# Kernel tuning notes

Hardware: AMD Instinct MI355X
Metric: run time of the kernel (lower is better)

## Reference

```python
import jax, jax.numpy as jnp
import numpy as np

B, N, DIN, DOUT = 4, 4096, 512, 128
NEG_INF = -1.0e9  # matches torch's -1000000000.0 fill


def setup_inputs() -> dict:
    key = jax.random.key(0)
    k1, k2, k3, k4 = jax.random.split(key, 4)
    x = jax.random.normal(k1, (B, N, DIN), dtype=jnp.float32)
    adj = (jax.random.uniform(k2, (N, N)) < 0.004).astype(jnp.float32)
    # xavier_uniform with gain=sqrt(2) for weights
    lim_w = float(np.sqrt(2.0) * np.sqrt(6.0 / (DIN + DOUT)))
    weights = jax.random.uniform(k3, (DIN, DOUT), jnp.float32, -lim_w, lim_w)
    # xavier_uniform (gain=1) for a: shape [2*DOUT, 1]
    lim_a = float(np.sqrt(6.0 / (2 * DOUT + 1)))
    a = jax.random.uniform(k4, (2 * DOUT, 1), jnp.float32, -lim_a, lim_a)
    return {"x": x, "adj": adj, "weights": weights, "a": a}


def reference(x, adj, weights, a):
    d = weights.shape[1]
    a_src = a[:d]   # [D, 1]
    a_dst = a[d:]   # [D, 1]

    def per_graph(xs):  # xs: [N, DIN]
        wh = xs @ weights                      # [N, D]
        e = wh @ a_src + (wh @ a_dst).T        # [N,1] + [1,N] -> [N,N]
        e = jnp.where(e > 0, e, 0.01 * e)      # LeakyReLU(0.01)
        att = jax.nn.softmax(jnp.where(adj > 0, e, NEG_INF), axis=1)
        out = att @ wh                          # [N, D]
        return adj @ out                        # sparse-adj mm (dense here)

    return jax.nn.relu(jax.vmap(per_graph)(x))  # act = ReLU
```

## Files before the change

### kernel.cpp

```cpp
#include <hip/hip_runtime.h>
#include <cstdint>
#include <cstddef>

#define BATCH 4
#define NNODE 4096
#define DIN   512
#define DOUT  128
#define CAP   64

typedef __attribute__((ext_vector_type(8))) short bf16x8;
typedef __attribute__((ext_vector_type(4))) float f32x4;
typedef __attribute__((ext_vector_type(4))) unsigned short us4;

static __device__ __forceinline__ unsigned short f2bf_rne(float f) {
    union { float f; uint32_t u; } v; v.f = f;
    uint32_t u = v.u;
    uint32_t r = u + 0x7FFFu + ((u >> 16) & 1u);
    return (unsigned short)(r >> 16);
}
static __device__ __forceinline__ float bf2f(unsigned short h) {
    union { float f; uint32_t u; } v; v.u = ((uint32_t)h) << 16;
    return v.f;
}

__global__ __launch_bounds__(256) void k_pre(const float* __restrict__ adj,
                                             const float* __restrict__ W,
                                             int* __restrict__ nbr_cnt,
                                             int* __restrict__ nbr_idx,
                                             unsigned short* __restrict__ Wt) {
    int t = threadIdx.x;
    if (blockIdx.x < NNODE) {
        __shared__ int scnt;
        int row = blockIdx.x;
        if (t == 0) scnt = 0;
        __syncthreads();
        const float4* p = (const float4*)(adj + (size_t)row * NNODE) + t * 4;
        unsigned mask = 0;
#pragma unroll
        for (int q = 0; q < 4; ++q) {
            float4 v = p[q];
            mask |= (v.x > 0.f ? 1u : 0u) << (q*4+0);
            mask |= (v.y > 0.f ? 1u : 0u) << (q*4+1);
            mask |= (v.z > 0.f ? 1u : 0u) << (q*4+2);
            mask |= (v.w > 0.f ? 1u : 0u) << (q*4+3);
        }
        int cnt = __popc(mask);
        int base = cnt ? atomicAdd(&scnt, cnt) : 0;
        int cbase = t * 16;
        while (mask) {
            int b = __ffs(mask) - 1;
            mask &= mask - 1;
            if (base < CAP) nbr_idx[row * CAP + base] = cbase + b;
            ++base;
        }
        __syncthreads();
        if (t == 0) nbr_cnt[row] = scnt > CAP ? CAP : scnt;
    } else {
        int wb = blockIdx.x - NNODE;
        int i0 = wb * 1024;
#pragma unroll
        for (int r = 0; r < 4; ++r) {
            int i = i0 + r * 256 + t;
            int n = i >> 9;
            int k = i & (DIN - 1);
            Wt[i] = f2bf_rne(W[(size_t)k * DOUT + n]);
        }
    }
}

__global__ __launch_bounds__(256) void k_wh(const float* __restrict__ x,
                                            const unsigned short* __restrict__ Wt,
                                            const float* __restrict__ a,
                                            unsigned short* __restrict__ wh,
                                            float* __restrict__ sv,
                                            float* __restrict__ dvv,
                                            float* __restrict__ colpart) {
    __shared__ float lacc[3][8][64][4];
    int t = threadIdx.x;
    int w = t >> 6;
    int l = t & 63;
    int rowbase = blockIdx.x * 16;
    int row = rowbase + (l & 15);
    int kq = w * 128 + ((l >> 4) << 3);
    f32x4 acc[8] = {};
    const float* xrow = x + (size_t)row * DIN + kq;
    const unsigned short* wb = Wt + kq;
#pragma unroll
    for (int ks = 0; ks < 4; ++ks) {
        float4 a0 = *(const float4*)(xrow + ks * 32);
        float4 a1 = *(const float4*)(xrow + ks * 32 + 4);
        float af[8] = {a0.x,a0.y,a0.z,a0.w,a1.x,a1.y,a1.z,a1.w};
        bf16x8 ah, al;
#pragma unroll
        for (int i = 0; i < 8; ++i) {
            unsigned short hh = f2bf_rne(af[i]);
            ah[i] = (short)hh;
            al[i] = (short)f2bf_rne(af[i] - bf2f(hh));
        }
#pragma unroll
        for (int ni = 0; ni < 8; ++ni) {
            bf16x8 b = *(const bf16x8*)(wb + (size_t)(ni*16 + (l & 15)) * DIN + ks * 32);
            acc[ni] = __builtin_amdgcn_mfma_f32_16x16x32_bf16(ah, b, acc[ni], 0, 0, 0);
            acc[ni] = __builtin_amdgcn_mfma_f32_16x16x32_bf16(al, b, acc[ni], 0, 0, 0);
        }
    }
    if (w > 0) {
#pragma unroll
        for (int ni = 0; ni < 8; ++ni)
            *(f32x4*)&lacc[w-1][ni][l][0] = acc[ni];
    }
    __syncthreads();
    if (w == 0) {
#pragma unroll
        for (int ni = 0; ni < 8; ++ni) {
            acc[ni] += *(const f32x4*)&lacc[0][ni][l][0];
            acc[ni] += *(const f32x4*)&lacc[1][ni][l][0];
            acc[ni] += *(const f32x4*)&lacc[2][ni][l][0];
        }
        float sp[4] = {0,0,0,0}, dp[4] = {0,0,0,0};
#pragma unroll
        for (int ni = 0; ni < 8; ++ni) {
            int col = ni*16 + (l & 15);
            float as = a[col], ad = a[DOUT + col];
#pragma unroll
            for (int r = 0; r < 4; ++r) {
                sp[r] += acc[ni][r] * as;
                dp[r] += acc[ni][r] * ad;
            }
        }
#pragma unroll
        for (int off = 1; off <= 8; off <<= 1) {
#pragma unroll
            for (int r = 0; r < 4; ++r) {
                sp[r] += __shfl_xor(sp[r], off, 64);
                dp[r] += __shfl_xor(dp[r], off, 64);
            }
        }
        int row4 = rowbase + ((l >> 4) << 2);
        if ((l & 15) == 0) {
#pragma unroll
            for (int r = 0; r < 4; ++r) {
                sv[row4 + r] = sp[r];
                dvv[row4 + r] = dp[r];
            }
        }
#pragma unroll
        for (int ni = 0; ni < 8; ++ni) {
            int col = ni*16 + (l & 15);
            float rs = acc[ni][0] + acc[ni][1] + acc[ni][2] + acc[ni][3];
            rs += __shfl_xor(rs, 16, 64);
            rs += __shfl_xor(rs, 32, 64);
            if (l < 16) colpart[(size_t)blockIdx.x * DOUT + ni*16 + l] = rs;
#pragma unroll
            for (int r = 0; r < 4; ++r)
                wh[(size_t)(row4 + r) * DOUT + col] = f2bf_rne(acc[ni][r]);
        }
    }
}

__global__ __launch_bounds__(256) void k_att(const unsigned short* __restrict__ wh,
                                             const float* __restrict__ s,
                                             const float* __restrict__ dv,
                                             const int* __restrict__ nbr_cnt,
                                             const int* __restrict__ nbr_idx,
                                             const float* __restrict__ colpart,
                                             unsigned short* __restrict__ out) {
    int bswz = (int)(((blockIdx.x & 7) << 9) | (blockIdx.x >> 3));
    int gid = bswz * 4 + (threadIdx.x >> 6);
    int l = threadIdx.x & 63;
    int b = gid >> 12;
    int i = gid & (NNODE - 1);
    int bb = b << 12;
    int c = nbr_cnt[i];
    int j = (l < c) ? nbr_idx[i * CAP + l] : 0;
    float p = 0.f;
    if (l < c) {
        float ev = s[gid] + dv[bb + j];
        ev = ev > 0.f ? ev : 0.01f * ev;
        p = __expf(ev);
    }
    float den = p;
#pragma unroll
    for (int off = 32; off >= 1; off >>= 1) den += __shfl_xor(den, off, 64);
    int half = l >> 5;
    int lc = l & 31;
    float4 acc = {0.f, 0.f, 0.f, 0.f};
    if (c > 0) {
        for (int jj = 0; jj < c; jj += 8) {
            int s0 = jj + half,     s1 = jj + 2 + half;
            int s2 = jj + 4 + half, s3 = jj + 6 + half;
            int jv0 = __shfl(j, s0, 64); float pv0 = __shfl(p, s0, 64);
            int jv1 = __shfl(j, s1, 64); float pv1 = __shfl(p, s1, 64);
            int jv2 = __shfl(j, s2, 64); float pv2 = __shfl(p, s2, 64);
            int jv3 = __shfl(j, s3, 64); float pv3 = __shfl(p, s3, 64);
            us4 v0 = *((const us4*)(wh + (size_t)(bb + jv0) * DOUT) + lc);
            us4 v1 = *((const us4*)(wh + (size_t)(bb + jv1) * DOUT) + lc);
            us4 v2 = *((const us4*)(wh + (size_t)(bb + jv2) * DOUT) + lc);
            us4 v3 = *((const us4*)(wh + (size_t)(bb + jv3) * DOUT) + lc);
            acc.x += pv0*bf2f(v0[0]) + pv1*bf2f(v1[0]) + pv2*bf2f(v2[0]) + pv3*bf2f(v3[0]);
            acc.y += pv0*bf2f(v0[1]) + pv1*bf2f(v1[1]) + pv2*bf2f(v2[1]) + pv3*bf2f(v3[1]);
            acc.z += pv0*bf2f(v0[2]) + pv1*bf2f(v1[2]) + pv2*bf2f(v2[2]) + pv3*bf2f(v3[2]);
            acc.w += pv0*bf2f(v0[3]) + pv1*bf2f(v1[3]) + pv2*bf2f(v2[3]) + pv3*bf2f(v3[3]);
        }
        acc.x += __shfl_xor(acc.x, 32, 64);
        acc.y += __shfl_xor(acc.y, 32, 64);
        acc.z += __shfl_xor(acc.z, 32, 64);
        acc.w += __shfl_xor(acc.w, 32, 64);
        float inv = 1.f / den;
        acc.x *= inv; acc.y *= inv; acc.z *= inv; acc.w *= inv;
    } else {
        const float inv_n = 1.f / (float)NNODE;
        for (int gg = 0; gg < 256; ++gg) {
            const float* cp = colpart + (size_t)((b << 8) + gg) * DOUT + lc*4;
            acc.x += cp[0]; acc.y += cp[1]; acc.z += cp[2]; acc.w += cp[3];
        }
        acc.x *= inv_n; acc.y *= inv_n; acc.z *= inv_n; acc.w *= inv_n;
    }
    if (half == 0) {
        us4 o;
        o[0] = f2bf_rne(acc.x); o[1] = f2bf_rne(acc.y);
        o[2] = f2bf_rne(acc.z); o[3] = f2bf_rne(acc.w);
        *((us4*)(out + (size_t)gid * DOUT) + lc) = o;
    }
}

__global__ __launch_bounds__(256) void k_agg(const unsigned short* __restrict__ out,
                                             const int* __restrict__ nbr_cnt,
                                             const int* __restrict__ nbr_idx,
                                             float* __restrict__ y) {
    int bswz = (int)(((blockIdx.x & 7) << 9) | (blockIdx.x >> 3));
    int gid = bswz * 4 + (threadIdx.x >> 6);
    int l = threadIdx.x & 63;
    int b = gid >> 12;
    int i = gid & (NNODE - 1);
    int bb = b << 12;
    int c = nbr_cnt[i];
    int j = (l < c) ? nbr_idx[i * CAP + l] : 0;
    float wt = (l < c) ? 1.f : 0.f;
    int half = l >> 5;
    int lc = l & 31;
    float4 acc = {0.f, 0.f, 0.f, 0.f};
    for (int jj = 0; jj < c; jj += 8) {
        int s0 = jj + half,     s1 = jj + 2 + half;
        int s2 = jj + 4 + half, s3 = jj + 6 + half;
        int jv0 = __shfl(j, s0, 64); float pv0 = __shfl(wt, s0, 64);
        int jv1 = __shfl(j, s1, 64); float pv1 = __shfl(wt, s1, 64);
        int jv2 = __shfl(j, s2, 64); float pv2 = __shfl(wt, s2, 64);
        int jv3 = __shfl(j, s3, 64); float pv3 = __shfl(wt, s3, 64);
        us4 v0 = *((const us4*)(out + (size_t)(bb + jv0) * DOUT) + lc);
        us4 v1 = *((const us4*)(out + (size_t)(bb + jv1) * DOUT) + lc);
        us4 v2 = *((const us4*)(out + (size_t)(bb + jv2) * DOUT) + lc);
        us4 v3 = *((const us4*)(out + (size_t)(bb + jv3) * DOUT) + lc);
        acc.x += pv0*bf2f(v0[0]) + pv1*bf2f(v1[0]) + pv2*bf2f(v2[0]) + pv3*bf2f(v3[0]);
        acc.y += pv0*bf2f(v0[1]) + pv1*bf2f(v1[1]) + pv2*bf2f(v2[1]) + pv3*bf2f(v3[1]);
        acc.z += pv0*bf2f(v0[2]) + pv1*bf2f(v1[2]) + pv2*bf2f(v2[2]) + pv3*bf2f(v3[2]);
        acc.w += pv0*bf2f(v0[3]) + pv1*bf2f(v1[3]) + pv2*bf2f(v2[3]) + pv3*bf2f(v3[3]);
    }
    acc.x += __shfl_xor(acc.x, 32, 64);
    acc.y += __shfl_xor(acc.y, 32, 64);
    acc.z += __shfl_xor(acc.z, 32, 64);
    acc.w += __shfl_xor(acc.w, 32, 64);
    acc.x = fmaxf(acc.x, 0.f); acc.y = fmaxf(acc.y, 0.f);
    acc.z = fmaxf(acc.z, 0.f); acc.w = fmaxf(acc.w, 0.f);
    if (half == 0)
        *((float4*)(y + (size_t)gid * DOUT) + lc) = acc;
}

extern "C" void kernel_launch(void* const* d_in, const int* in_sizes, int n_in,
                              void* d_out, int out_size, void* d_ws, size_t ws_size,
                              hipStream_t stream) {
    const float* x   = (const float*)d_in[0];
    const float* adj = (const float*)d_in[1];
    const float* W   = (const float*)d_in[2];
    const float* a   = (const float*)d_in[3];
    float* y = (float*)d_out;

    char* ws = (char*)d_ws;
    size_t o = 0;
    int*            nbr_cnt = (int*)(ws + o);            o += (size_t)NNODE * 4;
    int*            nbr_idx = (int*)(ws + o);            o += (size_t)NNODE * CAP * 4;
    unsigned short* Wt      = (unsigned short*)(ws + o); o += (size_t)DOUT * DIN * 2;
    unsigned short* wh      = (unsigned short*)(ws + o); o += (size_t)BATCH * NNODE * DOUT * 2;
    float*          sv      = (float*)(ws + o);          o += (size_t)BATCH * NNODE * 4;
    float*          dvv     = (float*)(ws + o);          o += (size_t)BATCH * NNODE * 4;
    float*          colpart = (float*)(ws + o);          o += (size_t)1024 * DOUT * 4;
    unsigned short* outbuf  = (unsigned short*)(ws + o); o += (size_t)BATCH * NNODE * DOUT * 2;

    k_pre<<<NNODE + 64, 256, 0, stream>>>(adj, W, nbr_cnt, nbr_idx, Wt);
    k_wh <<<1024, 256, 0, stream>>>(x, Wt, a, wh, sv, dvv, colpart);
    k_att<<<(BATCH*NNODE)/4, 256, 0, stream>>>(wh, sv, dvv, nbr_cnt, nbr_idx, colpart, outbuf);
    k_agg<<<(BATCH*NNODE)/4, 256, 0, stream>>>(outbuf, nbr_cnt, nbr_idx, y);
}
```

Before: 162.6 us.

## Fuse adjacency scan with Wh GEMM in one interleaved kernel

Splits the weight transpose into its own small kernel and merges the adjacency neighbor-list build with the x@W GEMM into one launch. Every fifth block does a GEMM tile and the other four scan one adjacency row, so bandwidth-bound and MFMA work run at the same time. The GEMM epilogue now spreads the wh/colpart writes across all four waves. The neighbor compaction replaces the shared atomic with a deterministic prefix scan, which costs many extra barriers per row block.

```diff
diff --git a/kernel.cpp b/kernel.cpp
--- a/kernel.cpp
+++ b/kernel.cpp
@@ -8,6 +8,8 @@
 #define DOUT  128
 #define CAP   64
 
+#define WH_BLOCKS 1024
+
 typedef __attribute__((ext_vector_type(8))) short bf16x8;
 typedef __attribute__((ext_vector_type(4))) float f32x4;
 typedef __attribute__((ext_vector_type(4))) unsigned short us4;
@@ -23,17 +25,118 @@
     return v.f;
 }
 
-__global__ __launch_bounds__(256) void k_pre(const float* __restrict__ adj,
-                                             const float* __restrict__ W,
-                                             int* __restrict__ nbr_cnt,
-                                             int* __restrict__ nbr_idx,
-                                             unsigned short* __restrict__ Wt) {
+__global__ __launch_bounds__(256) void k_wt(const float* __restrict__ W,
+                                            unsigned short* __restrict__ Wt) {
     int t = threadIdx.x;
-    if (blockIdx.x < NNODE) {
-        __shared__ int scnt;
-        int row = blockIdx.x;
-        if (t == 0) scnt = 0;
+    int i0 = blockIdx.x * 1024;
+#pragma unroll
+    for (int r = 0; r < 4; ++r) {
+        int i = i0 + r * 256 + t;
+        int n = i >> 9;
+        int k = i & (DIN - 1);
+        Wt[i] = f2bf_rne(W[(size_t)k * DOUT + n]);
+    }
+}
+
+__global__ __launch_bounds__(256) void k_main(const float* __restrict__ x,
+                                              const float* __restrict__ adj,
+                                              const unsigned short* __restrict__ Wt,
+                                              const float* __restrict__ a,
+                                              unsigned short* __restrict__ wh,
+                                              float* __restrict__ sv,
+                                              float* __restrict__ dvv,
+                                              float* __restrict__ colpart,
+                                              int* __restrict__ nbr_cnt,
+                                              int* __restrict__ nbr_idx) {
+    __shared__ float lacc[4][8][64][4];
+    __shared__ int pref[256];
+    int t = threadIdx.x;
+    int w = t >> 6;
+    int l = t & 63;
+    int bid = blockIdx.x;
+
+    if (bid % 5 == 0) {
+        int rowbase = (bid / 5) * 16;
+        int row = rowbase + (l & 15);
+        int kq = w * 128 + ((l >> 4) << 3);
+        f32x4 acc[8] = {};
+        const float* xrow = x + (size_t)row * DIN + kq;
+        const unsigned short* wb = Wt + kq;
+#pragma unroll
+        for (int ks = 0; ks < 4; ++ks) {
+            float4 a0 = *(const float4*)(xrow + ks * 32);
+            float4 a1 = *(const float4*)(xrow + ks * 32 + 4);
+            float af[8] = {a0.x,a0.y,a0.z,a0.w,a1.x,a1.y,a1.z,a1.w};
+            bf16x8 ah, al;
+#pragma unroll
+            for (int i = 0; i < 8; ++i) {
+                unsigned short hh = f2bf_rne(af[i]);
+                ah[i] = (short)hh;
+                al[i] = (short)f2bf_rne(af[i] - bf2f(hh));
+            }
+#pragma unroll
+            for (int ni = 0; ni < 8; ++ni) {
+                bf16x8 b = *(const bf16x8*)(wb + (size_t)(ni*16 + (l & 15)) * DIN + ks * 32);
+                acc[ni] = __builtin_amdgcn_mfma_f32_16x16x32_bf16(ah, b, acc[ni], 0, 0, 0);
+                acc[ni] = __builtin_amdgcn_mfma_f32_16x16x32_bf16(al, b, acc[ni], 0, 0, 0);
+            }
+        }
+#pragma unroll
+        for (int ni = 0; ni < 8; ++ni)
+            *(f32x4*)&lacc[w][ni][l][0] = acc[ni];
         __syncthreads();
+
+        int row4 = rowbase + ((l >> 4) << 2);
+#pragma unroll
+        for (int q = 0; q < 2; ++q) {
+            int ni = w * 2 + q;
+            f32x4 sum = *(const f32x4*)&lacc[0][ni][l][0];
+            sum += *(const f32x4*)&lacc[1][ni][l][0];
+            sum += *(const f32x4*)&lacc[2][ni][l][0];
+            sum += *(const f32x4*)&lacc[3][ni][l][0];
+            int col = ni*16 + (l & 15);
+#pragma unroll
+            for (int r = 0; r < 4; ++r)
+                wh[(size_t)(row4 + r) * DOUT + col] = f2bf_rne(sum[r]);
+            float rs = sum[0] + sum[1] + sum[2] + sum[3];
+            rs += __shfl_xor(rs, 16, 64);
+            rs += __shfl_xor(rs, 32, 64);
+            if (l < 16) colpart[(size_t)(bid / 5) * DOUT + ni*16 + l] = rs;
+        }
+        if (w == 0) {
+            float sp[4] = {0,0,0,0}, dp[4] = {0,0,0,0};
+#pragma unroll
+            for (int ni = 0; ni < 8; ++ni) {
+                f32x4 sum = *(const f32x4*)&lacc[0][ni][l][0];
+                sum += *(const f32x4*)&lacc[1][ni][l][0];
+                sum += *(const f32x4*)&lacc[2][ni][l][0];
+                sum += *(const f32x4*)&lacc[3][ni][l][0];
+                int col = ni*16 + (l & 15);
+                float as = a[col], ad = a[DOUT + col];
+#pragma unroll
+                for (int r = 0; r < 4; ++r) {
+                    sp[r] += sum[r] * as;
+                    dp[r] += sum[r] * ad;
+                }
+            }
+#pragma unroll
+            for (int off = 1; off <= 8; off <<= 1) {
+#pragma unroll
+                for (int r = 0; r < 4; ++r) {
+                    sp[r] += __shfl_xor(sp[r], off, 64);
+                    dp[r] += __shfl_xor(dp[r], off, 64);
+                }
+            }
+            if ((l & 15) == 0) {
+#pragma unroll
+                for (int r = 0; r < 4; ++r) {
+                    sv[row4 + r] = sp[r];
+                    dvv[row4 + r] = dp[r];
+                }
+            }
+        }
+    } else {
+        int row = bid - bid / 5 - 1;
         const float4* p = (const float4*)(adj + (size_t)row * NNODE) + t * 4;
         unsigned mask = 0;
 #pragma unroll
@@ -45,7 +148,17 @@
             mask |= (v.w > 0.f ? 1u : 0u) << (q*4+3);
         }
         int cnt = __popc(mask);
-        int base = cnt ? atomicAdd(&scnt, cnt) : 0;
+        pref[t] = cnt;
+        __syncthreads();
+        for (int off = 1; off < 256; off <<= 1) {
+            int v = pref[t];
+            int add = (t >= off) ? pref[t - off] : 0;
+            __syncthreads();
+            pref[t] = v + add;
+            __syncthreads();
+        }
+        int total = pref[255];
+        int base = pref[t] - cnt;
         int cbase = t * 16;
         while (mask) {
             int b = __ffs(mask) - 1;
@@ -53,108 +166,7 @@
             if (base < CAP) nbr_idx[row * CAP + base] = cbase + b;
             ++base;
         }
-        __syncthreads();
-        if (t == 0) nbr_cnt[row] = scnt > CAP ? CAP : scnt;
-    } else {
-        int wb = blockIdx.x - NNODE;
-        int i0 = wb * 1024;
-#pragma unroll
-        for (int r = 0; r < 4; ++r) {
-            int i = i0 + r * 256 + t;
-            int n = i >> 9;
-            int k = i & (DIN - 1);
-            Wt[i] = f2bf_rne(W[(size_t)k * DOUT + n]);
-        }
-    }
-}
-
-__global__ __launch_bounds__(256) void k_wh(const float* __restrict__ x,
-                                            const unsigned short* __restrict__ Wt,
-                                            const float* __restrict__ a,
-                                            unsigned short* __restrict__ wh,
-                                            float* __restrict__ sv,
-                                            float* __restrict__ dvv,
-                                            float* __restrict__ colpart) {
-    __shared__ float lacc[3][8][64][4];
-    int t = threadIdx.x;
-    int w = t >> 6;
-    int l = t & 63;
-    int rowbase = blockIdx.x * 16;
-    int row = rowbase + (l & 15);
-    int kq = w * 128 + ((l >> 4) << 3);
-    f32x4 acc[8] = {};
-    const float* xrow = x + (size_t)row * DIN + kq;
-    const unsigned short* wb = Wt + kq;
-#pragma unroll
-    for (int ks = 0; ks < 4; ++ks) {
-        float4 a0 = *(const float4*)(xrow + ks * 32);
-        float4 a1 = *(const float4*)(xrow + ks * 32 + 4);
-        float af[8] = {a0.x,a0.y,a0.z,a0.w,a1.x,a1.y,a1.z,a1.w};
-        bf16x8 ah, al;
-#pragma unroll
-        for (int i = 0; i < 8; ++i) {
-            unsigned short hh = f2bf_rne(af[i]);
-            ah[i] = (short)hh;
-            al[i] = (short)f2bf_rne(af[i] - bf2f(hh));
-        }
-#pragma unroll
-        for (int ni = 0; ni < 8; ++ni) {
-            bf16x8 b = *(const bf16x8*)(wb + (size_t)(ni*16 + (l & 15)) * DIN + ks * 32);
-            acc[ni] = __builtin_amdgcn_mfma_f32_16x16x32_bf16(ah, b, acc[ni], 0, 0, 0);
-            acc[ni] = __builtin_amdgcn_mfma_f32_16x16x32_bf16(al, b, acc[ni], 0, 0, 0);
-        }
-    }
-    if (w > 0) {
-#pragma unroll
-        for (int ni = 0; ni < 8; ++ni)
-            *(f32x4*)&lacc[w-1][ni][l][0] = acc[ni];
-    }
-    __syncthreads();
-    if (w == 0) {
-#pragma unroll
-        for (int ni = 0; ni < 8; ++ni) {
-            acc[ni] += *(const f32x4*)&lacc[0][ni][l][0];
-            acc[ni] += *(const f32x4*)&lacc[1][ni][l][0];
-            acc[ni] += *(const f32x4*)&lacc[2][ni][l][0];
-        }
-        float sp[4] = {0,0,0,0}, dp[4] = {0,0,0,0};
-#pragma unroll
-        for (int ni = 0; ni < 8; ++ni) {
-            int col = ni*16 + (l & 15);
-            float as = a[col], ad = a[DOUT + col];
-#pragma unroll
-            for (int r = 0; r < 4; ++r) {
-                sp[r] += acc[ni][r] * as;
-                dp[r] += acc[ni][r] * ad;
-            }
-        }
-#pragma unroll
-        for (int off = 1; off <= 8; off <<= 1) {
-#pragma unroll
-            for (int r = 0; r < 4; ++r) {
-                sp[r] += __shfl_xor(sp[r], off, 64);
-                dp[r] += __shfl_xor(dp[r], off, 64);
-            }
-        }
-        int row4 = rowbase + ((l >> 4) << 2);
-        if ((l & 15) == 0) {
-#pragma unroll
-            for (int r = 0; r < 4; ++r) {
-                sv[row4 + r] = sp[r];
-                dvv[row4 + r] = dp[r];
-            }
-        }
-#pragma unroll
-        for (int ni = 0; ni < 8; ++ni) {
-            int col = ni*16 + (l & 15);
-            float rs = acc[ni][0] + acc[ni][1] + acc[ni][2] + acc[ni][3];
-            rs += __shfl_xor(rs, 16, 64);
-            rs += __shfl_xor(rs, 32, 64);
-            if (l < 16) colpart[(size_t)blockIdx.x * DOUT + ni*16 + l] = rs;
-#pragma unroll
-            for (int r = 0; r < 4; ++r)
-                wh[(size_t)(row4 + r) * DOUT + col] = f2bf_rne(acc[ni][r]);
-        }
+        if (t == 0) nbr_cnt[row] = total > CAP ? CAP : total;
     }
 }
 
@@ -283,11 +295,12 @@
     unsigned short* wh      = (unsigned short*)(ws + o); o += (size_t)BATCH * NNODE * DOUT * 2;
     float*          sv      = (float*)(ws + o);          o += (size_t)BATCH * NNODE * 4;
     float*          dvv     = (float*)(ws + o);          o += (size_t)BATCH * NNODE * 4;
-    float*          colpart = (float*)(ws + o);          o += (size_t)1024 * DOUT * 4;
+    float*          colpart = (float*)(ws + o);          o += (size_t)WH_BLOCKS * DOUT * 4;
     unsigned short* outbuf  = (unsigned short*)(ws + o); o += (size_t)BATCH * NNODE * DOUT * 2;
 
-    k_pre<<<NNODE + 64, 256, 0, stream>>>(adj, W, nbr_cnt, nbr_idx, Wt);
-    k_wh <<<1024, 256, 0, stream>>>(x, Wt, a, wh, sv, dvv, colpart);
-    k_att<<<(BATCH*NNODE)/4, 256, 0, stream>>>(wh, sv, dvv, nbr_cnt, nbr_idx, colpart, outbuf);
-    k_agg<<<(BATCH*NNODE)/4, 256, 0, stream>>>(outbuf, nbr_cnt, nbr_idx, y);
-}
+    k_wt  <<<64, 256, 0, stream>>>(W, Wt);
+    k_main<<<WH_BLOCKS + NNODE, 256, 0, stream>>>(x, adj, Wt, a, wh, sv, dvv,
+                                                  colpart, nbr_cnt, nbr_idx);
+    k_att <<<(BATCH*NNODE)/4, 256, 0, stream>>>(wh, sv, dvv, nbr_cnt, nbr_idx, colpart, outbuf);
+    k_agg <<<(BATCH*NNODE)/4, 256, 0, stream>>>(outbuf, nbr_cnt, nbr_idx, y);
+}
```

After: 169.8 us. +4.4%, slower.
